# Performance work log

Hardware: AMD Instinct MI355X
Metric: run time of the kernel (lower is better)

## Reference

```python
import jax, jax.numpy as jnp
import numpy as np

N = 100000
E = 1280000
D = 64


def setup_inputs() -> dict:
    key = jax.random.key(0)
    k1, k2, k3, k4, k5, k6 = jax.random.split(key, 6)
    return {
        "x": jax.random.normal(k1, (N, D), dtype=jnp.float32),
        "w_src": jax.random.normal(k2, (D,), dtype=jnp.float32),
        "w_dst": jax.random.normal(k3, (D,), dtype=jnp.float32),
        "ew": jax.random.normal(k4, (E,), dtype=jnp.float32),
        "src_idx": jax.random.randint(k5, (E,), 0, N, dtype=jnp.int64),
        "dst_idx": jax.random.randint(k6, (E,), 0, N, dtype=jnp.int64),
    }


def reference(x, w_src, w_dst, ew, src_idx, dst_idx):
    # Per-node scalar scores: Linear(emb_dim, 1, bias=False)
    a_src = x @ w_src            # [N]
    a_dst = x @ w_dst            # [N]
    # Edge attention: tanh(a_src[u] + a_dst[v]) * ew  (u_add_v + tanh + scale)
    a = jnp.tanh(a_src[src_idx] + a_dst[dst_idx]) * ew   # [E]
    # Message = a_e * x[src_e]; reduce = scatter-sum over dst (u_mul_e + sum)
    m = a[:, None] * x[src_idx]                           # [E, D]
    h = jax.ops.segment_sum(m, dst_idx, num_segments=N)   # [N, D]
    return h
```

## Files before the change

### kernel.cpp

```cpp
#include <hip/hip_runtime.h>
#include <hip/hip_fp16.h>
#include <math.h>

#define DIM  64
#define SPAN 256
#define NBIN 256
#define KMAX 512
#define CAP  6144

__global__ void score_kernel(const float* __restrict__ x,
                             const float* __restrict__ w_src,
                             const float* __restrict__ w_dst,
                             float* __restrict__ a_src,
                             float* __restrict__ a_dst,
                             __half* __restrict__ xh,
                             int N) {
    int gid  = blockIdx.x * blockDim.x + threadIdx.x;
    int node = gid >> 6;
    int lane = threadIdx.x & 63;
    if (node >= N) return;
    float xv = x[(size_t)node * DIM + lane];
    xh[(size_t)node * DIM + lane] = __float2half_rn(xv);
    float s1 = xv * w_src[lane];
    float s2 = xv * w_dst[lane];
    #pragma unroll
    for (int off = 32; off > 0; off >>= 1) {
        s1 += __shfl_down(s1, off, 64);
        s2 += __shfl_down(s2, off, 64);
    }
    if (lane == 0) {
        a_src[node] = s1;
        a_dst[node] = s2;
    }
}

__global__ __launch_bounds__(1024) void hist_coarse(
        const int* __restrict__ dst, int* __restrict__ cnt,
        int E, int N, int K) {
    __shared__ int lh[KMAX];
    int tid = threadIdx.x;
    for (int j = tid; j < K; j += blockDim.x) lh[j] = 0;
    __syncthreads();
    for (int base = blockIdx.x * 1024; base < E; base += NBIN * 1024) {
        int e = base + tid;
        if (e < E) {
            unsigned t = (unsigned)dst[e];
            if (t >= (unsigned)N) t = 0;
            atomicAdd(&lh[t >> 8], 1);
        }
    }
    __syncthreads();
    for (int j = tid; j < K; j += blockDim.x)
        cnt[j * NBIN + blockIdx.x] = lh[j];
}

__global__ void scan_part(const int* __restrict__ cnt, int* __restrict__ offs,
                          int* __restrict__ bsum, int N) {
    __shared__ int buf[2][256];
    int tid = threadIdx.x;
    int i = blockIdx.x * 256 + tid;
    int v = (i < N) ? cnt[i] : 0;
    int sel = 0;
    buf[0][tid] = v;
    __syncthreads();
    for (int off = 1; off < 256; off <<= 1) {
        int nsel = sel ^ 1;
        buf[nsel][tid] = buf[sel][tid] + ((tid >= off) ? buf[sel][tid - off] : 0);
        __syncthreads();
        sel = nsel;
    }
    if (i < N) offs[i] = buf[sel][tid] - v;
    if (tid == 255) bsum[blockIdx.x] = buf[sel][255];
}

__global__ void scan_top(int* __restrict__ bsum, int* __restrict__ offs,
                         int NB, int N) {
    __shared__ int buf[2][512];
    int tid = threadIdx.x;
    int v = (tid < NB) ? bsum[tid] : 0;
    int sel = 0;
    buf[0][tid] = v;
    __syncthreads();
    for (int off = 1; off < 512; off <<= 1) {
        int nsel = sel ^ 1;
        buf[nsel][tid] = buf[sel][tid] + ((tid >= off) ? buf[sel][tid - off] : 0);
        __syncthreads();
        sel = nsel;
    }
    if (tid < NB) bsum[tid] = buf[sel][tid] - v;
    if (tid == 511) offs[N] = buf[sel][511];
}

__global__ __launch_bounds__(1024) void binpass_kernel(
        const float* __restrict__ ew,
        const int* __restrict__ src_idx,
        const int* __restrict__ dst_idx,
        const float* __restrict__ a_src,
        const float* __restrict__ a_dst,
        const int* __restrict__ moffs,
        const int* __restrict__ bsum,
        unsigned long long* __restrict__ pay,
        int E, int N, int K) {
    __shared__ int lcur[KMAX];
    int tid = threadIdx.x;
    for (int j = tid; j < K; j += blockDim.x) {
        int i = j * NBIN + blockIdx.x;
        lcur[j] = moffs[i] + bsum[i >> 8];
    }
    __syncthreads();
    for (int base = blockIdx.x * 1024; base < E; base += NBIN * 1024) {
        int e = base + tid;
        if (e < E) {
            unsigned s = (unsigned)src_idx[e];
            unsigned t = (unsigned)dst_idx[e];
            if (s >= (unsigned)N) s = 0;
            if (t >= (unsigned)N) t = 0;
            float a = tanhf(a_src[s] + a_dst[t]) * ew[e];
            int bk = (int)(t >> 8);
            int pos = atomicAdd(&lcur[bk], 1);
            unsigned rec = (s << 8) | (t & 255u);
            pay[pos] = ((unsigned long long)rec << 32) |
                       (unsigned long long)__float_as_uint(a);
        }
    }
}

__global__ __launch_bounds__(1024) void sort_gather_kernel(
        const __half* __restrict__ xh,
        const float* __restrict__ x32,
        const unsigned long long* __restrict__ pay,
        const int* __restrict__ moffs,
        const int* __restrict__ bsum,
        float* __restrict__ h,
        int N, int K, int E) {
    __shared__ unsigned long long srec[CAP];
    __shared__ unsigned short sidx[CAP];
    __shared__ int hcnt[SPAN];
    __shared__ int hoff[2][SPAN];
    __shared__ int lcur[SPAN];
    __shared__ int nstart[SPAN];
    int tid = threadIdx.x;
    int b   = blockIdx.x;
    int i0 = b * NBIN;
    int bstart = moffs[i0] + bsum[i0 >> 8];
    int bend;
    if (b == K - 1) bend = E;
    else { int i1 = (b + 1) * NBIN; bend = moffs[i1] + bsum[i1 >> 8]; }
    int cnt = bend - bstart;

    if (cnt <= CAP) {
        if (tid < SPAN) hcnt[tid] = 0;
        __syncthreads();
        for (int i = tid; i < cnt; i += 1024) {
            unsigned long long r = pay[bstart + i];
            srec[i] = r;
            atomicAdd(&hcnt[(int)((r >> 32) & 255u)], 1);
        }
        __syncthreads();
        int sel = 0;
        if (tid < SPAN) hoff[0][tid] = hcnt[tid];
        __syncthreads();
        for (int off = 1; off < SPAN; off <<= 1) {
            int nsel = sel ^ 1;
            if (tid < SPAN)
                hoff[nsel][tid] = hoff[sel][tid] +
                                  ((tid >= off) ? hoff[sel][tid - off] : 0);
            __syncthreads();
            sel = nsel;
        }
        if (tid < SPAN) {
            int excl = hoff[sel][tid] - hcnt[tid];
            nstart[tid] = excl;
            lcur[tid]   = excl;
        }
        __syncthreads();
        for (int i = tid; i < cnt; i += 1024) {
            unsigned long long r = srec[i];
            int d = (int)((r >> 32) & 255u);
            int pos = atomicAdd(&lcur[d], 1);
            sidx[pos] = (unsigned short)i;
        }
        __syncthreads();
        int lane = tid & 63;
        int wave = tid >> 6;
        for (int d = wave; d < SPAN; d += 16) {
            int node = b * SPAN + d;
            if (node >= N) break;
            int p  = nstart[d];
            int pe = p + hcnt[d];
            float a0 = 0.f, a1 = 0.f, a2 = 0.f, a3 = 0.f;
            while (p + 8 <= pe) {
                unsigned long long r0 = srec[sidx[p]];
                unsigned long long r1 = srec[sidx[p + 1]];
                unsigned long long r2 = srec[sidx[p + 2]];
                unsigned long long r3 = srec[sidx[p + 3]];
                unsigned long long r4 = srec[sidx[p + 4]];
                unsigned long long r5 = srec[sidx[p + 5]];
                unsigned long long r6 = srec[sidx[p + 6]];
                unsigned long long r7 = srec[sidx[p + 7]];
                p += 8;
                unsigned s0 = (unsigned)(r0 >> 40); if (s0 >= (unsigned)N) s0 = 0;
                unsigned s1 = (unsigned)(r1 >> 40); if (s1 >= (unsigned)N) s1 = 0;
                unsigned s2 = (unsigned)(r2 >> 40); if (s2 >= (unsigned)N) s2 = 0;
                unsigned s3 = (unsigned)(r3 >> 40); if (s3 >= (unsigned)N) s3 = 0;
                unsigned s4 = (unsigned)(r4 >> 40); if (s4 >= (unsigned)N) s4 = 0;
                unsigned s5 = (unsigned)(r5 >> 40); if (s5 >= (unsigned)N) s5 = 0;
                unsigned s6 = (unsigned)(r6 >> 40); if (s6 >= (unsigned)N) s6 = 0;
                unsigned s7 = (unsigned)(r7 >> 40); if (s7 >= (unsigned)N) s7 = 0;
                float x0 = __half2float(xh[(size_t)s0 * DIM + lane]);
                float x1 = __half2float(xh[(size_t)s1 * DIM + lane]);
                float x2 = __half2float(xh[(size_t)s2 * DIM + lane]);
                float x3 = __half2float(xh[(size_t)s3 * DIM + lane]);
                float x4 = __half2float(xh[(size_t)s4 * DIM + lane]);
                float x5 = __half2float(xh[(size_t)s5 * DIM + lane]);
                float x6 = __half2float(xh[(size_t)s6 * DIM + lane]);
                float x7 = __half2float(xh[(size_t)s7 * DIM + lane]);
                a0 = fmaf(__uint_as_float((unsigned)r0), x0, a0);
                a1 = fmaf(__uint_as_float((unsigned)r1), x1, a1);
                a2 = fmaf(__uint_as_float((unsigned)r2), x2, a2);
                a3 = fmaf(__uint_as_float((unsigned)r3), x3, a3);
                a0 = fmaf(__uint_as_float((unsigned)r4), x4, a0);
                a1 = fmaf(__uint_as_float((unsigned)r5), x5, a1);
                a2 = fmaf(__uint_as_float((unsigned)r6), x6, a2);
                a3 = fmaf(__uint_as_float((unsigned)r7), x7, a3);
            }
            if (p + 4 <= pe) {
                unsigned long long r0 = srec[sidx[p]];
                unsigned long long r1 = srec[sidx[p + 1]];
                unsigned long long r2 = srec[sidx[p + 2]];
                unsigned long long r3 = srec[sidx[p + 3]];
                p += 4;
                unsigned s0 = (unsigned)(r0 >> 40); if (s0 >= (unsigned)N) s0 = 0;
                unsigned s1 = (unsigned)(r1 >> 40); if (s1 >= (unsigned)N) s1 = 0;
                unsigned s2 = (unsigned)(r2 >> 40); if (s2 >= (unsigned)N) s2 = 0;
                unsigned s3 = (unsigned)(r3 >> 40); if (s3 >= (unsigned)N) s3 = 0;
                float x0 = __half2float(xh[(size_t)s0 * DIM + lane]);
                float x1 = __half2float(xh[(size_t)s1 * DIM + lane]);
                float x2 = __half2float(xh[(size_t)s2 * DIM + lane]);
                float x3 = __half2float(xh[(size_t)s3 * DIM + lane]);
                a0 = fmaf(__uint_as_float((unsigned)r0), x0, a0);
                a1 = fmaf(__uint_as_float((unsigned)r1), x1, a1);
                a2 = fmaf(__uint_as_float((unsigned)r2), x2, a2);
                a3 = fmaf(__uint_as_float((unsigned)r3), x3, a3);
            }
            if (p + 2 <= pe) {
                unsigned long long r0 = srec[sidx[p]];
                unsigned long long r1 = srec[sidx[p + 1]];
                p += 2;
                unsigned s0 = (unsigned)(r0 >> 40); if (s0 >= (unsigned)N) s0 = 0;
                unsigned s1 = (unsigned)(r1 >> 40); if (s1 >= (unsigned)N) s1 = 0;
                a0 = fmaf(__uint_as_float((unsigned)r0),
                          __half2float(xh[(size_t)s0 * DIM + lane]), a0);
                a1 = fmaf(__uint_as_float((unsigned)r1),
                          __half2float(xh[(size_t)s1 * DIM + lane]), a1);
            }
            if (p < pe) {
                unsigned long long r0 = srec[sidx[p]];
                unsigned s0 = (unsigned)(r0 >> 40); if (s0 >= (unsigned)N) s0 = 0;
                a0 = fmaf(__uint_as_float((unsigned)r0),
                          __half2float(xh[(size_t)s0 * DIM + lane]), a0);
            }
            h[(size_t)node * DIM + lane] = (a0 + a1) + (a2 + a3);
        }
    } else {
        for (int j = tid; j < SPAN * DIM; j += 1024) {
            int node = b * SPAN + (j >> 6);
            if (node < N) h[(size_t)node * DIM + (j & 63)] = 0.f;
        }
        __syncthreads();
        for (int i = tid; i < cnt; i += 1024) {
            unsigned long long r = pay[bstart + i];
            unsigned s = (unsigned)(r >> 40);
            if (s >= (unsigned)N) s = 0;
            int node = b * SPAN + (int)((r >> 32) & 255u);
            float a = __uint_as_float((unsigned)r);
            if (node < N)
                for (int k = 0; k < DIM; ++k)
                    atomicAdd(&h[(size_t)node * DIM + k],
                              a * x32[(size_t)s * DIM + k]);
        }
    }
}

__global__ void zero_h_kernel(float* __restrict__ p, int n) {
    int i = blockIdx.x * blockDim.x + threadIdx.x;
    if (i < n) p[i] = 0.f;
}

__global__ void edge_kernel_atomic(const float* __restrict__ x,
                                   const float* __restrict__ ew,
                                   const int* __restrict__ src_idx,
                                   const int* __restrict__ dst_idx,
                                   const float* __restrict__ a_src,
                                   const float* __restrict__ a_dst,
                                   float* __restrict__ h,
                                   int E) {
    int gid  = blockIdx.x * blockDim.x + threadIdx.x;
    int e    = gid >> 6;
    int lane = threadIdx.x & 63;
    if (e >= E) return;
    int s = src_idx[e];
    int t = dst_idx[e];
    float a  = tanhf(a_src[s] + a_dst[t]) * ew[e];
    float xv = x[(size_t)s * DIM + lane];
    atomicAdd(&h[(size_t)t * DIM + lane], a * xv);
}

__global__ void score_only_kernel(const float* __restrict__ x,
                                  const float* __restrict__ w_src,
                                  const float* __restrict__ w_dst,
                                  float* __restrict__ a_src,
                                  float* __restrict__ a_dst,
                                  int N) {
    int gid  = blockIdx.x * blockDim.x + threadIdx.x;
    int node = gid >> 6;
    int lane = threadIdx.x & 63;
    if (node >= N) return;
    float xv = x[(size_t)node * DIM + lane];
    float s1 = xv * w_src[lane];
    float s2 = xv * w_dst[lane];
    #pragma unroll
    for (int off = 32; off > 0; off >>= 1) {
        s1 += __shfl_down(s1, off, 64);
        s2 += __shfl_down(s2, off, 64);
    }
    if (lane == 0) {
        a_src[node] = s1;
        a_dst[node] = s2;
    }
}

extern "C" void kernel_launch(void* const* d_in, const int* in_sizes, int n_in,
                              void* d_out, int out_size, void* d_ws, size_t ws_size,
                              hipStream_t stream) {
    const float* x     = (const float*)d_in[0];
    const float* w_src = (const float*)d_in[1];
    const float* w_dst = (const float*)d_in[2];
    const float* ew    = (const float*)d_in[3];
    const int*   src   = (const int*)d_in[4];
    const int*   dst   = (const int*)d_in[5];
    float* h = (float*)d_out;

    int N = in_sizes[0] / DIM;
    int E = in_sizes[3];

    int K    = (N + SPAN - 1) / SPAN;
    int Ntot = K * NBIN;
    int NBs  = (Ntot + 255) / 256;

    float* a_src  = (float*)d_ws;
    float* a_dst  = a_src + N;
    int*   moffs  = (int*)(a_dst + N);
    int*   bsum   = moffs + Ntot + 1;
    size_t head_bytes = ((size_t)(2 * N) + (size_t)Ntot + 1 + (size_t)NBs) * 4;
    size_t pay_off = (head_bytes + 15) & ~(size_t)15;
    unsigned long long* pay = (unsigned long long*)((char*)d_ws + pay_off);
    size_t xh_off = pay_off + (size_t)E * 8;
    __half* xh = (__half*)((char*)d_ws + xh_off);
    size_t need = xh_off + (size_t)N * DIM * 2;

    int score_blocks = (N + 3) / 4;

    if (ws_size < need || K > KMAX || NBs > 512 || (N * DIM) % 2 != 0) {
        score_only_kernel<<<score_blocks, 256, 0, stream>>>(x, w_src, w_dst,
                                                            a_src, a_dst, N);
        int ob = (out_size + 255) / 256;
        zero_h_kernel<<<ob, 256, 0, stream>>>(h, out_size);
        int edge_blocks = (E + 3) / 4;
        edge_kernel_atomic<<<edge_blocks, 256, 0, stream>>>(x, ew, src, dst,
                                                            a_src, a_dst, h, E);
        return;
    }

    score_kernel<<<score_blocks, 256, 0, stream>>>(x, w_src, w_dst,
                                                   a_src, a_dst, xh, N);
    hist_coarse<<<NBIN, 1024, 0, stream>>>(dst, moffs, E, N, K);
    scan_part<<<NBs, 256, 0, stream>>>(moffs, moffs, bsum, Ntot);
    scan_top<<<1, 512, 0, stream>>>(bsum, moffs, NBs, Ntot);
    binpass_kernel<<<NBIN, 1024, 0, stream>>>(ew, src, dst, a_src, a_dst,
                                              moffs, bsum, pay, E, N, K);
    sort_gather_kernel<<<K, 1024, 0, stream>>>(xh, x, pay, moffs, bsum,
                                               h, N, K, E);
}
```

Before: 185.9 us.

## Halve dst bin span and move attention compute into the gather stage

The destination bucket span drops from 256 to 128 nodes, which doubles the number of bins and blocks in the sort/gather stage and halves the per-block shared-memory capacity. The scan is widened to 512-element blocks. The tanh attention computation moves out of the binning pass into the gather kernel. There each wave loads 64 edge records cooperatively, computes the coefficients once per lane, and broadcasts source index and weight with shuffles. This cuts random a_src/a_dst reads from the binning pass and raises parallelism in the gather, at the cost of shuffle overhead and possibly more blocks overflowing the smaller capacity into the slow atomic path.

```diff
diff --git a/kernel.cpp b/kernel.cpp
--- a/kernel.cpp
+++ b/kernel.cpp
@@ -2,11 +2,12 @@
 #include <hip/hip_fp16.h>
 #include <math.h>
 
-#define DIM  64
-#define SPAN 256
-#define NBIN 256
-#define KMAX 512
-#define CAP  6144
+#define DIM   64
+#define SPAN  128
+#define SHIFT 7
+#define NBIN  256
+#define KMAX  1024
+#define CAP   3072
 
 __global__ void score_kernel(const float* __restrict__ x,
                              const float* __restrict__ w_src,
@@ -46,7 +47,7 @@
         if (e < E) {
             unsigned t = (unsigned)dst[e];
             if (t >= (unsigned)N) t = 0;
-            atomicAdd(&lh[t >> 8], 1);
+            atomicAdd(&lh[t >> SHIFT], 1);
         }
     }
     __syncthreads();
@@ -54,27 +55,26 @@
         cnt[j * NBIN + blockIdx.x] = lh[j];
 }
 
-__global__ void scan_part(const int* __restrict__ cnt, int* __restrict__ offs,
-                          int* __restrict__ bsum, int N) {
-    __shared__ int buf[2][256];
-    int tid = threadIdx.x;
-    int i = blockIdx.x * 256 + tid;
-    int v = (i < N) ? cnt[i] : 0;
+__global__ __launch_bounds__(512) void scan_part(int* __restrict__ data,
+                                                 int* __restrict__ bsum, int n) {
+    __shared__ int buf[2][512];
+    int tid = threadIdx.x;
+    int i = blockIdx.x * 512 + tid;
+    int v = (i < n) ? data[i] : 0;
     int sel = 0;
     buf[0][tid] = v;
     __syncthreads();
-    for (int off = 1; off < 256; off <<= 1) {
+    for (int off = 1; off < 512; off <<= 1) {
         int nsel = sel ^ 1;
         buf[nsel][tid] = buf[sel][tid] + ((tid >= off) ? buf[sel][tid - off] : 0);
         __syncthreads();
         sel = nsel;
     }
-    if (i < N) offs[i] = buf[sel][tid] - v;
-    if (tid == 255) bsum[blockIdx.x] = buf[sel][255];
-}
-
-__global__ void scan_top(int* __restrict__ bsum, int* __restrict__ offs,
-                         int NB, int N) {
+    if (i < n) data[i] = buf[sel][tid] - v;
+    if (tid == 511) bsum[blockIdx.x] = buf[sel][511];
+}
+
+__global__ __launch_bounds__(512) void scan_top(int* __restrict__ bsum, int NB) {
     __shared__ int buf[2][512];
     int tid = threadIdx.x;
     int v = (tid < NB) ? bsum[tid] : 0;
@@ -88,15 +88,12 @@
         sel = nsel;
     }
     if (tid < NB) bsum[tid] = buf[sel][tid] - v;
-    if (tid == 511) offs[N] = buf[sel][511];
 }
 
 __global__ __launch_bounds__(1024) void binpass_kernel(
         const float* __restrict__ ew,
         const int* __restrict__ src_idx,
         const int* __restrict__ dst_idx,
-        const float* __restrict__ a_src,
-        const float* __restrict__ a_dst,
         const int* __restrict__ moffs,
         const int* __restrict__ bsum,
         unsigned long long* __restrict__ pay,
@@ -105,7 +102,7 @@
     int tid = threadIdx.x;
     for (int j = tid; j < K; j += blockDim.x) {
         int i = j * NBIN + blockIdx.x;
-        lcur[j] = moffs[i] + bsum[i >> 8];
+        lcur[j] = moffs[i] + bsum[i >> 9];
     }
     __syncthreads();
     for (int base = blockIdx.x * 1024; base < E; base += NBIN * 1024) {
@@ -115,12 +112,11 @@
             unsigned t = (unsigned)dst_idx[e];
             if (s >= (unsigned)N) s = 0;
             if (t >= (unsigned)N) t = 0;
-            float a = tanhf(a_src[s] + a_dst[t]) * ew[e];
-            int bk = (int)(t >> 8);
+            int bk = (int)(t >> SHIFT);
             int pos = atomicAdd(&lcur[bk], 1);
-            unsigned rec = (s << 8) | (t & 255u);
+            unsigned rec = (s << 8) | (t & (SPAN - 1));
             pay[pos] = ((unsigned long long)rec << 32) |
-                       (unsigned long long)__float_as_uint(a);
+                       (unsigned long long)__float_as_uint(ew[e]);
         }
     }
 }
@@ -128,6 +124,8 @@
 __global__ __launch_bounds__(1024) void sort_gather_kernel(
         const __half* __restrict__ xh,
         const float* __restrict__ x32,
+        const float* __restrict__ a_src,
+        const float* __restrict__ a_dst,
         const unsigned long long* __restrict__ pay,
         const int* __restrict__ moffs,
         const int* __restrict__ bsum,
@@ -142,10 +140,10 @@
     int tid = threadIdx.x;
     int b   = blockIdx.x;
     int i0 = b * NBIN;
-    int bstart = moffs[i0] + bsum[i0 >> 8];
+    int bstart = moffs[i0] + bsum[i0 >> 9];
     int bend;
     if (b == K - 1) bend = E;
-    else { int i1 = (b + 1) * NBIN; bend = moffs[i1] + bsum[i1 >> 8]; }
+    else { int i1 = (b + 1) * NBIN; bend = moffs[i1] + bsum[i1 >> 9]; }
     int cnt = bend - bstart;
 
     if (cnt <= CAP) {
@@ -154,7 +152,7 @@
         for (int i = tid; i < cnt; i += 1024) {
             unsigned long long r = pay[bstart + i];
             srec[i] = r;
-            atomicAdd(&hcnt[(int)((r >> 32) & 255u)], 1);
+            atomicAdd(&hcnt[(int)((r >> 32) & (SPAN - 1))], 1);
         }
         __syncthreads();
         int sel = 0;
@@ -176,7 +174,7 @@
         __syncthreads();
         for (int i = tid; i < cnt; i += 1024) {
             unsigned long long r = srec[i];
-            int d = (int)((r >> 32) & 255u);
+            int d = (int)((r >> 32) & (SPAN - 1));
             int pos = atomicAdd(&lcur[d], 1);
             sidx[pos] = (unsigned short)i;
         }
@@ -186,81 +184,56 @@
         for (int d = wave; d < SPAN; d += 16) {
             int node = b * SPAN + d;
             if (node >= N) break;
-            int p  = nstart[d];
-            int pe = p + hcnt[d];
-            float a0 = 0.f, a1 = 0.f, a2 = 0.f, a3 = 0.f;
-            while (p + 8 <= pe) {
-                unsigned long long r0 = srec[sidx[p]];
-                unsigned long long r1 = srec[sidx[p + 1]];
-                unsigned long long r2 = srec[sidx[p + 2]];
-                unsigned long long r3 = srec[sidx[p + 3]];
-                unsigned long long r4 = srec[sidx[p + 4]];
-                unsigned long long r5 = srec[sidx[p + 5]];
-                unsigned long long r6 = srec[sidx[p + 6]];
-                unsigned long long r7 = srec[sidx[p + 7]];
-                p += 8;
-                unsigned s0 = (unsigned)(r0 >> 40); if (s0 >= (unsigned)N) s0 = 0;
-                unsigned s1 = (unsigned)(r1 >> 40); if (s1 >= (unsigned)N) s1 = 0;
-                unsigned s2 = (unsigned)(r2 >> 40); if (s2 >= (unsigned)N) s2 = 0;
-                unsigned s3 = (unsigned)(r3 >> 40); if (s3 >= (unsigned)N) s3 = 0;
-                unsigned s4 = (unsigned)(r4 >> 40); if (s4 >= (unsigned)N) s4 = 0;
-                unsigned s5 = (unsigned)(r5 >> 40); if (s5 >= (unsigned)N) s5 = 0;
-                unsigned s6 = (unsigned)(r6 >> 40); if (s6 >= (unsigned)N) s6 = 0;
-                unsigned s7 = (unsigned)(r7 >> 40); if (s7 >= (unsigned)N) s7 = 0;
-                float x0 = __half2float(xh[(size_t)s0 * DIM + lane]);
-                float x1 = __half2float(xh[(size_t)s1 * DIM + lane]);
-                float x2 = __half2float(xh[(size_t)s2 * DIM + lane]);
-                float x3 = __half2float(xh[(size_t)s3 * DIM + lane]);
-                float x4 = __half2float(xh[(size_t)s4 * DIM + lane]);
-                float x5 = __half2float(xh[(size_t)s5 * DIM + lane]);
-                float x6 = __half2float(xh[(size_t)s6 * DIM + lane]);
-                float x7 = __half2float(xh[(size_t)s7 * DIM + lane]);
-                a0 = fmaf(__uint_as_float((unsigned)r0), x0, a0);
-                a1 = fmaf(__uint_as_float((unsigned)r1), x1, a1);
-                a2 = fmaf(__uint_as_float((unsigned)r2), x2, a2);
-                a3 = fmaf(__uint_as_float((unsigned)r3), x3, a3);
-                a0 = fmaf(__uint_as_float((unsigned)r4), x4, a0);
-                a1 = fmaf(__uint_as_float((unsigned)r5), x5, a1);
-                a2 = fmaf(__uint_as_float((unsigned)r6), x6, a2);
-                a3 = fmaf(__uint_as_float((unsigned)r7), x7, a3);
+            int p   = nstart[d];
+            int deg = hcnt[d];
+            float adt = a_dst[node];
+            float acc0 = 0.f, acc1 = 0.f, acc2 = 0.f, acc3 = 0.f;
+            for (int c0 = 0; c0 < deg; c0 += 64) {
+                int m = deg - c0; if (m > 64) m = 64;
+                float aL = 0.f; unsigned sL = 0;
+                if (lane < m) {
+                    unsigned long long r = srec[sidx[p + c0 + lane]];
+                    unsigned s = (unsigned)(r >> 40);
+                    if (s >= (unsigned)N) s = 0;
+                    aL = tanhf(a_src[s] + adt) * __uint_as_float((unsigned)r);
+                    sL = s;
+                }
+                for (int j = 0; j < m; j += 8) {
+                    unsigned s0 = (unsigned)__shfl((int)sL, j + 0, 64);
+                    unsigned s1 = (unsigned)__shfl((int)sL, j + 1, 64);
+                    unsigned s2 = (unsigned)__shfl((int)sL, j + 2, 64);
+                    unsigned s3 = (unsigned)__shfl((int)sL, j + 3, 64);
+                    unsigned s4 = (unsigned)__shfl((int)sL, j + 4, 64);
+                    unsigned s5 = (unsigned)__shfl((int)sL, j + 5, 64);
+                    unsigned s6 = (unsigned)__shfl((int)sL, j + 6, 64);
+                    unsigned s7 = (unsigned)__shfl((int)sL, j + 7, 64);
+                    float b0 = __shfl(aL, j + 0, 64);
+                    float b1 = __shfl(aL, j + 1, 64);
+                    float b2 = __shfl(aL, j + 2, 64);
+                    float b3 = __shfl(aL, j + 3, 64);
+                    float b4 = __shfl(aL, j + 4, 64);
+                    float b5 = __shfl(aL, j + 5, 64);
+                    float b6 = __shfl(aL, j + 6, 64);
+                    float b7 = __shfl(aL, j + 7, 64);
+                    float x0 = __half2float(xh[(size_t)s0 * DIM + lane]);
+                    float x1 = __half2float(xh[(size_t)s1 * DIM + lane]);
+                    float x2 = __half2float(xh[(size_t)s2 * DIM + lane]);
+                    float x3 = __half2float(xh[(size_t)s3 * DIM + lane]);
+                    float x4 = __half2float(xh[(size_t)s4 * DIM + lane]);
+                    float x5 = __half2float(xh[(size_t)s5 * DIM + lane]);
+                    float x6 = __half2float(xh[(size_t)s6 * DIM + lane]);
+                    float x7 = __half2float(xh[(size_t)s7 * DIM + lane]);
+                    acc0 = fmaf(b0, x0, acc0);
+                    acc1 = fmaf(b1, x1, acc1);
+                    acc2 = fmaf(b2, x2, acc2);
+                    acc3 = fmaf(b3, x3, acc3);
+                    acc0 = fmaf(b4, x4, acc0);
+                    acc1 = fmaf(b5, x5, acc1);
+                    acc2 = fmaf(b6, x6, acc2);
+                    acc3 = fmaf(b7, x7, acc3);
+                }
             }
-            if (p + 4 <= pe) {
-                unsigned long long r0 = srec[sidx[p]];
-                unsigned long long r1 = srec[sidx[p + 1]];
-                unsigned long long r2 = srec[sidx[p + 2]];
-                unsigned long long r3 = srec[sidx[p + 3]];
-                p += 4;
-                unsigned s0 = (unsigned)(r0 >> 40); if (s0 >= (unsigned)N) s0 = 0;
-                unsigned s1 = (unsigned)(r1 >> 40); if (s1 >= (unsigned)N) s1 = 0;
-                unsigned s2 = (unsigned)(r2 >> 40); if (s2 >= (unsigned)N) s2 = 0;
-                unsigned s3 = (unsigned)(r3 >> 40); if (s3 >= (unsigned)N) s3 = 0;
-                float x0 = __half2float(xh[(size_t)s0 * DIM + lane]);
-                float x1 = __half2float(xh[(size_t)s1 * DIM + lane]);
-                float x2 = __half2float(xh[(size_t)s2 * DIM + lane]);
-                float x3 = __half2float(xh[(size_t)s3 * DIM + lane]);
-                a0 = fmaf(__uint_as_float((unsigned)r0), x0, a0);
-                a1 = fmaf(__uint_as_float((unsigned)r1), x1, a1);
-                a2 = fmaf(__uint_as_float((unsigned)r2), x2, a2);
-                a3 = fmaf(__uint_as_float((unsigned)r3), x3, a3);
-            }
-            if (p + 2 <= pe) {
-                unsigned long long r0 = srec[sidx[p]];
-                unsigned long long r1 = srec[sidx[p + 1]];
-                p += 2;
-                unsigned s0 = (unsigned)(r0 >> 40); if (s0 >= (unsigned)N) s0 = 0;
-                unsigned s1 = (unsigned)(r1 >> 40); if (s1 >= (unsigned)N) s1 = 0;
-                a0 = fmaf(__uint_as_float((unsigned)r0),
-                          __half2float(xh[(size_t)s0 * DIM + lane]), a0);
-                a1 = fmaf(__uint_as_float((unsigned)r1),
-                          __half2float(xh[(size_t)s1 * DIM + lane]), a1);
-            }
-            if (p < pe) {
-                unsigned long long r0 = srec[sidx[p]];
-                unsigned s0 = (unsigned)(r0 >> 40); if (s0 >= (unsigned)N) s0 = 0;
-                a0 = fmaf(__uint_as_float((unsigned)r0),
-                          __half2float(xh[(size_t)s0 * DIM + lane]), a0);
-            }
-            h[(size_t)node * DIM + lane] = (a0 + a1) + (a2 + a3);
+            h[(size_t)node * DIM + lane] = (acc0 + acc1) + (acc2 + acc3);
         }
     } else {
         for (int j = tid; j < SPAN * DIM; j += 1024) {
@@ -272,12 +245,14 @@
             unsigned long long r = pay[bstart + i];
             unsigned s = (unsigned)(r >> 40);
             if (s >= (unsigned)N) s = 0;
-            int node = b * SPAN + (int)((r >> 32) & 255u);
-            float a = __uint_as_float((unsigned)r);
-            if (node < N)
+            int node = b * SPAN + (int)((r >> 32) & (SPAN - 1));
+            if (node < N) {
+                float a = tanhf(a_src[s] + a_dst[node]) *
+                          __uint_as_float((unsigned)r);
                 for (int k = 0; k < DIM; ++k)
                     atomicAdd(&h[(size_t)node * DIM + k],
                               a * x32[(size_t)s * DIM + k]);
+            }
         }
     }
 }
@@ -346,7 +321,7 @@
 
     int K    = (N + SPAN - 1) / SPAN;
     int Ntot = K * NBIN;
-    int NBs  = (Ntot + 255) / 256;
+    int NBs  = (Ntot + 511) / 512;
 
     float* a_src  = (float*)d_ws;
     float* a_dst  = a_src + N;
@@ -361,7 +336,7 @@
 
     int score_blocks = (N + 3) / 4;
 
-    if (ws_size < need || K > KMAX || NBs > 512 || (N * DIM) % 2 != 0) {
+    if (ws_size < need || K > KMAX || NBs > 512 || N >= (1 << 24)) {
         score_only_kernel<<<score_blocks, 256, 0, stream>>>(x, w_src, w_dst,
                                                             a_src, a_dst, N);
         int ob = (out_size + 255) / 256;
@@ -375,10 +350,10 @@
     score_kernel<<<score_blocks, 256, 0, stream>>>(x, w_src, w_dst,
                                                    a_src, a_dst, xh, N);
     hist_coarse<<<NBIN, 1024, 0, stream>>>(dst, moffs, E, N, K);
-    scan_part<<<NBs, 256, 0, stream>>>(moffs, moffs, bsum, Ntot);
-    scan_top<<<1, 512, 0, stream>>>(bsum, moffs, NBs, Ntot);
-    binpass_kernel<<<NBIN, 1024, 0, stream>>>(ew, src, dst, a_src, a_dst,
-                                              moffs, bsum, pay, E, N, K);
-    sort_gather_kernel<<<K, 1024, 0, stream>>>(xh, x, pay, moffs, bsum,
-                                               h, N, K, E);
-}
+    scan_part<<<NBs, 512, 0, stream>>>(moffs, bsum, Ntot);
+    scan_top<<<1, 512, 0, stream>>>(bsum, NBs);
+    binpass_kernel<<<NBIN, 1024, 0, stream>>>(ew, src, dst, moffs, bsum,
+                                              pay, E, N, K);
+    sort_gather_kernel<<<K, 1024, 0, stream>>>(xh, x, a_src, a_dst, pay,
+                                               moffs, bsum, h, N, K, E);
+}
```

Measured after the change: 192.5 us. 3.5% more time.
